# Performance work log

Measured on AMD Instinct MI355X. Metric: run time of the kernel, lower is better.

Reference implementation:

```python
import jax, jax.numpy as jnp
import numpy as np

NUM_HEADS = 4
NUM_GROUPS = 32
EPS = 1e-5

def setup_inputs() -> dict:
    key = jax.random.key(0)
    ks = jax.random.split(key, 3)
    B, C, H, W = 4, 256, 64, 64
    x = jax.random.normal(ks[0], (B, C, H, W), jnp.float32)
    gn_w = jnp.ones((C,), jnp.float32)
    gn_b = jnp.zeros((C,), jnp.float32)
    qkv_w = jax.random.normal(ks[1], (3 * C, C), jnp.float32) * 0.02
    qkv_b = jnp.zeros((3 * C,), jnp.float32)
    proj_w = jax.random.normal(ks[2], (C, C), jnp.float32) * 0.02
    proj_b = jnp.zeros((C,), jnp.float32)
    return dict(x=x, gn_w=gn_w, gn_b=gn_b, qkv_w=qkv_w, qkv_b=qkv_b,
                proj_w=proj_w, proj_b=proj_b)

def reference(x, gn_w, gn_b, qkv_w, qkv_b, proj_w, proj_b):
    B, C, H, W = x.shape
    n = H * W
    xf = x.reshape(B, C, n)
    # GroupNorm(32, C) over (channels-in-group, n)
    xg = xf.reshape(B, NUM_GROUPS, -1)
    mu = xg.mean(-1, keepdims=True)
    var = xg.var(-1, keepdims=True)
    xn = ((xg - mu) * jax.lax.rsqrt(var + EPS)).reshape(B, C, n)
    xn = xn * gn_w[None, :, None] + gn_b[None, :, None]
    # 1x1 conv QKV: [B, 3C, n]
    qkv = jnp.einsum('oc,bcn->bon', qkv_w, xn) + qkv_b[None, :, None]
    # head split exactly as torch: reshape(B*heads, 3C//heads, n) then chunk
    qkv = qkv.reshape(B * NUM_HEADS, 3 * C // NUM_HEADS, n)
    q, k, v = jnp.split(qkv, 3, axis=1)  # each [B*heads, head_dim, n]
    scale = (C // NUM_HEADS) ** -0.25
    w = jnp.einsum('bct,bcs->bts', q * scale, k * scale)  # [B*heads, n, n]
    w = jax.nn.softmax(w, axis=-1)
    h = jnp.einsum('bts,bcs->bct', w, v).reshape(B, C, n)
    h = jnp.einsum('oc,bcn->bon', proj_w, h) + proj_b[None, :, None]
    return x + h.reshape(B, C, H, W)
```

## Files before the change

### kernel.cpp

```cpp
#include <hip/hip_runtime.h>

typedef unsigned short u16;
typedef unsigned int u32;
typedef __bf16 bf16x8 __attribute__((ext_vector_type(8)));
typedef float f32x4 __attribute__((ext_vector_type(4)));
typedef u16 u16x4 __attribute__((ext_vector_type(4)));
typedef u16 u16x8 __attribute__((ext_vector_type(8)));

#define MFMA16x16x32(a, b, c) __builtin_amdgcn_mfma_f32_16x16x32_bf16((a), (b), (c), 0, 0, 0)

static constexpr int kB = 4;
static constexpr int kC = 256;
static constexpr int kN = 4096;
static constexpr int kHeads = 4;
static constexpr int kD = 64;
static constexpr int kSplit = 2;
static constexpr float kScale = 0.35355339059327373f;
static constexpr float kScaleQ = 0.51006971545f;

__device__ __forceinline__ u16 f2bf(float f) {
  union { float f; u32 i; } v; v.f = f;
  return (u16)((v.i + 0x7fffu + ((v.i >> 16) & 1u)) >> 16);
}
__device__ __forceinline__ bf16x8 ldb8(const u16* p) {
  return *reinterpret_cast<const bf16x8*>(p);
}
__device__ __forceinline__ float fast_exp2(float x) {
#if __has_builtin(__builtin_amdgcn_exp2f)
  return __builtin_amdgcn_exp2f(x);
#else
  float r;
  asm("v_exp_f32 %0, %1" : "=v"(r) : "v"(x));
  return r;
#endif
}

__global__ void convert_bf16(const float* __restrict__ in, u16* __restrict__ out,
                             int n) {
  for (int i = blockIdx.x * blockDim.x + threadIdx.x; i < n;
       i += gridDim.x * blockDim.x)
    out[i] = f2bf(in[i]);
}

__global__ __launch_bounds__(1024) void gn_kernel(const float* __restrict__ x,
                                                  const float* __restrict__ gnw,
                                                  const float* __restrict__ gnb,
                                                  u16* __restrict__ xnT) {
  const int g = blockIdx.x, b = blockIdx.y;
  const int tid = threadIdx.x;
  const float* xb = x + b * (kC * kN) + g * 8 * kN;
  float vals[4][8];
  float s = 0.f, ss = 0.f;
#pragma unroll
  for (int kk = 0; kk < 4; ++kk) {
    const int t = tid + kk * 1024;
#pragma unroll
    for (int c = 0; c < 8; ++c) {
      const float v_ = xb[c * kN + t];
      vals[kk][c] = v_;
      s += v_; ss += v_ * v_;
    }
  }
#pragma unroll
  for (int off = 32; off > 0; off >>= 1) {
    s += __shfl_down(s, off);
    ss += __shfl_down(ss, off);
  }
  __shared__ float rbuf[32];
  const int wid = tid >> 6, lane = tid & 63;
  if (lane == 0) { rbuf[wid] = s; rbuf[16 + wid] = ss; }
  __syncthreads();
  if (tid < 64) {
    float s2 = (lane < 16) ? rbuf[lane] : 0.f;
    float ss2 = (lane < 16) ? rbuf[16 + lane] : 0.f;
#pragma unroll
    for (int off = 8; off > 0; off >>= 1) {
      s2 += __shfl_down(s2, off);
      ss2 += __shfl_down(ss2, off);
    }
    if (lane == 0) { rbuf[0] = s2; rbuf[1] = ss2; }
  }
  __syncthreads();
  const float inv_n = 1.f / 32768.f;
  const float mu = rbuf[0] * inv_n;
  const float var = rbuf[1] * inv_n - mu * mu;
  const float rs = rsqrtf(var + 1e-5f);
  float wv[8], bv[8];
#pragma unroll
  for (int c = 0; c < 8; ++c) {
    const float wgt = gnw[g * 8 + c] * rs;
    wv[c] = wgt;
    bv[c] = gnb[g * 8 + c] - mu * wgt;
  }
  u16* ob = xnT + b * (kN * kC) + g * 8;
#pragma unroll
  for (int kk = 0; kk < 4; ++kk) {
    const int t = tid + kk * 1024;
    u16x8 pk;
#pragma unroll
    for (int c = 0; c < 8; ++c) pk[c] = f2bf(vals[kk][c] * wv[c] + bv[c]);
    *reinterpret_cast<u16x8*>(ob + t * kC) = pk;
  }
}

__global__ __launch_bounds__(256) void qkv_gemm(const u16* __restrict__ qkvw,
                                                const float* __restrict__ qkvb,
                                                const u16* __restrict__ xnT,
                                                u16* __restrict__ qt,
                                                u16* __restrict__ kt,
                                                u16* __restrict__ vv) {
  const int nblk = blockIdx.x, mblk = blockIdx.y, b = blockIdx.z;
  const int tid = threadIdx.x;
  const int w = tid >> 6, l = tid & 63, quad = l >> 4, col = l & 15;
  const int m0 = mblk * 64 + w * 16;
  const int n0 = nblk * 64;
  __shared__ __align__(16) u16 als[64 * 256];
  __shared__ __align__(16) u16 bls[64 * 256];
  {
    const u16* asrc = qkvw + (size_t)(mblk * 64) * kC;
    const u16* bsrc = xnT + (size_t)b * (kN * kC) + (size_t)n0 * kC;
#pragma unroll
    for (int p = 0; p < 8; ++p) {
      const int li = p * 256 + tid;
      const int row = li >> 5, ch = li & 31;
      const int sw = (ch ^ (row & 7)) * 8;
      *reinterpret_cast<bf16x8*>(&als[row * 256 + sw]) = ldb8(asrc + li * 8);
      *reinterpret_cast<bf16x8*>(&bls[row * 256 + sw]) = ldb8(bsrc + li * 8);
    }
  }
  __syncthreads();
  f32x4 acc[4] = {{0,0,0,0},{0,0,0,0},{0,0,0,0},{0,0,0,0}};
  const u16* arow = &als[(w * 16 + col) * 256];
  const int kx = col & 7;
#pragma unroll
  for (int ks = 0; ks < 8; ++ks) {
    const bf16x8 af = ldb8(arow + (((ks * 4 + quad) ^ kx)) * 8);
#pragma unroll
    for (int nt = 0; nt < 4; ++nt) {
      const bf16x8 bfr =
          ldb8(&bls[(nt * 16 + col) * 256 + (((ks * 4 + quad) ^ kx)) * 8]);
      acc[nt] = MFMA16x16x32(af, bfr, acc[nt]);
    }
  }
  const int o_base = m0 + quad * 4;
  const int head = o_base / 192;
  const int rr = o_base % 192;
  const int bh = b * kHeads + head;
  const int seg = rr >> 6;
  const int c0 = rr & 63;
  float bias[4];
#pragma unroll
  for (int r = 0; r < 4; ++r) bias[r] = qkvb[o_base + r];
  const float sc = (seg == 0) ? kScaleQ : kScale;
#pragma unroll
  for (int nt = 0; nt < 4; ++nt) {
    const int t = n0 + nt * 16 + col;
    if (seg == 2) {
      const int tp = n0 + (nt >> 1) * 32 + 8 * (col >> 2) + 4 * (nt & 1) + (col & 3);
#pragma unroll
      for (int r = 0; r < 4; ++r)
        vv[bh * (kD * kN) + (c0 + r) * kN + tp] = f2bf(acc[nt][r] + bias[r]);
    } else {
      u16* dst = (seg == 0 ? qt : kt) + bh * (kN * kD) + t * kD + c0;
      u16x4 pk;
#pragma unroll
      for (int r = 0; r < 4; ++r) pk[r] = f2bf((acc[nt][r] + bias[r]) * sc);
      *reinterpret_cast<u16x4*>(dst) = pk;
    }
  }
}

__global__ __launch_bounds__(256, 2) void attn_split(const u16* __restrict__ qt,
                                                     const u16* __restrict__ kt,
                                                     const u16* __restrict__ vv,
                                                     float* __restrict__ pO,
                                                     float* __restrict__ pl) {
  const int tblk = blockIdx.x, bh = blockIdx.y, z = blockIdx.z;
  const int tid = threadIdx.x;
  const int w = tid >> 6, l = tid & 63, quad = l >> 4, col = l & 15;
  const int t0 = tblk * 256 + w * 64;
  const u16* qb = qt + bh * (kN * kD);
  const u16* kb = kt + bh * (kN * kD);
  const u16* vb = vv + bh * (kD * kN);
  bf16x8 qf[4][2];
#pragma unroll
  for (int ti = 0; ti < 4; ++ti) {
    qf[ti][0] = ldb8(qb + (t0 + ti * 16 + col) * kD + quad * 8);
    qf[ti][1] = ldb8(qb + (t0 + ti * 16 + col) * kD + 32 + quad * 8);
  }
  u16x8 ones_u;
#pragma unroll
  for (int i = 0; i < 8; ++i) ones_u[i] = 0x3f80;
  const bf16x8 onesf = *reinterpret_cast<bf16x8*>(&ones_u);
  f32x4 oacc[4][4];
  f32x4 lacc[4];
#pragma unroll
  for (int ti = 0; ti < 4; ++ti) {
    lacc[ti] = f32x4{0, 0, 0, 0};
#pragma unroll
    for (int ct = 0; ct < 4; ++ct) oacc[ti][ct] = f32x4{0, 0, 0, 0};
  }

  __shared__ __align__(16) u16 kls[2][32][64];
  __shared__ __align__(16) u16 vls[2][32][64];
  constexpr int NIT = (kN / kSplit) / 32;
  const int s_beg = z * (kN / kSplit);

  const int srow = tid >> 3, sk8 = tid & 7, skey = srow & 7;
  const u16* ksrc = kb + (size_t)(s_beg + srow) * kD + sk8 * 8;
  u16* kdst = &kls[0][srow][((sk8 ^ skey)) * 8];
  const int sa = sk8 >> 2, sq = sk8 & 3;
  const u16* vsrc = vb + (size_t)(2 * srow + sa) * kN + s_beg + sq * 8;
  u16* vdst = &vls[0][srow][(((sa << 2) | sq) ^ skey) * 8];

  bf16x8 kstg = ldb8(ksrc);
  bf16x8 vstg = ldb8(vsrc);

#pragma unroll 2
  for (int it = 0; it < NIT; ++it) {
    const int cb = (it & 1) * (32 * 64);
    *reinterpret_cast<bf16x8*>(kdst + cb) = kstg;
    *reinterpret_cast<bf16x8*>(vdst + cb) = vstg;
    __syncthreads();
    if (it + 1 < NIT) {
      kstg = ldb8(ksrc + (size_t)(it + 1) * (32 * kD));
      vstg = ldb8(vsrc + (it + 1) * 32);
    }
    const u16* kl = &kls[0][0][0] + cb;
    const u16* vl = &vls[0][0][0] + cb;
    const int kx = (col & 7) * 8;
    const bf16x8 k00 = ldb8(kl + col * 64 + ((quad * 8) ^ kx));
    const bf16x8 k01 = ldb8(kl + col * 64 + ((32 + quad * 8) ^ kx));
    const bf16x8 k10 = ldb8(kl + (col + 16) * 64 + ((quad * 8) ^ kx));
    const bf16x8 k11 = ldb8(kl + (col + 16) * 64 + ((32 + quad * 8) ^ kx));
    bf16x8 vf[4];
    const int vslot = (((col & 1) << 2) | quad) ^ (col >> 1);
#pragma unroll
    for (int ct = 0; ct < 4; ++ct)
      vf[ct] = ldb8(vl + (ct * 8 + (col >> 1)) * 64 + vslot * 8);
#pragma unroll
    for (int ti = 0; ti < 4; ++ti) {
      f32x4 sa0 = {0, 0, 0, 0}, sa1 = {0, 0, 0, 0};
      sa0 = MFMA16x16x32(k00, qf[ti][0], sa0);
      sa0 = MFMA16x16x32(k01, qf[ti][1], sa0);
      sa1 = MFMA16x16x32(k10, qf[ti][0], sa1);
      sa1 = MFMA16x16x32(k11, qf[ti][1], sa1);
      const u32 e00 = __float_as_uint(fast_exp2(sa0[0]));
      const u32 e01 = __float_as_uint(fast_exp2(sa0[1]));
      const u32 e02 = __float_as_uint(fast_exp2(sa0[2]));
      const u32 e03 = __float_as_uint(fast_exp2(sa0[3]));
      const u32 e10 = __float_as_uint(fast_exp2(sa1[0]));
      const u32 e11 = __float_as_uint(fast_exp2(sa1[1]));
      const u32 e12 = __float_as_uint(fast_exp2(sa1[2]));
      const u32 e13 = __float_as_uint(fast_exp2(sa1[3]));
      union { u32 wd[4]; bf16x8 v; } pa;
      pa.wd[0] = __builtin_amdgcn_perm(e01, e00, 0x07060302u);
      pa.wd[1] = __builtin_amdgcn_perm(e03, e02, 0x07060302u);
      pa.wd[2] = __builtin_amdgcn_perm(e11, e10, 0x07060302u);
      pa.wd[3] = __builtin_amdgcn_perm(e13, e12, 0x07060302u);
#pragma unroll
      for (int ct = 0; ct < 4; ++ct)
        oacc[ti][ct] = MFMA16x16x32(pa.v, vf[ct], oacc[ti][ct]);
      lacc[ti] = MFMA16x16x32(pa.v, onesf, lacc[ti]);
    }
  }
  float* po = pO + (size_t)(z * 16 + bh) * kN * kD;
  float* plp = pl + (size_t)(z * 16 + bh) * kN;
#pragma unroll
  for (int ti = 0; ti < 4; ++ti)
#pragma unroll
    for (int r = 0; r < 4; ++r) {
      const int t = t0 + ti * 16 + quad * 4 + r;
#pragma unroll
      for (int ct = 0; ct < 4; ++ct)
        po[(size_t)t * kD + ct * 16 + col] = oacc[ti][ct][r];
      if (col == 0) plp[t] = lacc[ti][r];
    }
}

__global__ __launch_bounds__(256) void attn_combine(const float* __restrict__ pO,
                                                    const float* __restrict__ pl,
                                                    u16* __restrict__ ht) {
  const int idx = blockIdx.x * 256 + threadIdx.x;
  const int c0 = (idx & 15) * 4;
  const int t = (idx >> 4) & (kN - 1);
  const int bh = idx >> 16;
  f32x4 acc = {0, 0, 0, 0};
  float lsum = 0.f;
#pragma unroll
  for (int z = 0; z < kSplit; ++z) {
    const size_t base = ((size_t)(z * 16 + bh) * kN + t);
    acc += *reinterpret_cast<const f32x4*>(pO + base * kD + c0);
    lsum += pl[base];
  }
  const float inv = 1.f / lsum;
  u16x4 pk;
#pragma unroll
  for (int i = 0; i < 4; ++i) pk[i] = f2bf(acc[i] * inv);
  const int b = bh >> 2, head = bh & 3;
  *reinterpret_cast<u16x4*>(ht + (size_t)b * (kN * kC) + (size_t)t * kC +
                            head * kD + c0) = pk;
}

__global__ __launch_bounds__(256) void proj_kernel(const u16* __restrict__ projw,
                                                   const float* __restrict__ projb,
                                                   const u16* __restrict__ ht,
                                                   const float* __restrict__ x,
                                                   float* __restrict__ out) {
  const int nblk = blockIdx.x, mblk = blockIdx.y, b = blockIdx.z;
  const int tid = threadIdx.x;
  const int w = tid >> 6, l = tid & 63, quad = l >> 4, col = l & 15;
  const int m0 = mblk * 64 + w * 16;
  const int n0 = nblk * 64;
  __shared__ __align__(16) u16 als[64 * 256];
  __shared__ __align__(16) u16 bls[64 * 256];
  {
    const u16* asrc = projw + (size_t)(mblk * 64) * kC;
    const u16* bsrc = ht + (size_t)b * (kN * kC) + (size_t)n0 * kC;
#pragma unroll
    for (int p = 0; p < 8; ++p) {
      const int li = p * 256 + tid;
      const int row = li >> 5, ch = li & 31;
      const int sw = (ch ^ (row & 7)) * 8;
      *reinterpret_cast<bf16x8*>(&als[row * 256 + sw]) = ldb8(asrc + li * 8);
      *reinterpret_cast<bf16x8*>(&bls[row * 256 + sw]) = ldb8(bsrc + li * 8);
    }
  }
  __syncthreads();
  f32x4 acc[4] = {{0,0,0,0},{0,0,0,0},{0,0,0,0},{0,0,0,0}};
  const u16* arow = &als[(w * 16 + col) * 256];
  const int kx = col & 7;
#pragma unroll
  for (int ks = 0; ks < 8; ++ks) {
    const bf16x8 af = ldb8(arow + (((ks * 4 + quad) ^ kx)) * 8);
#pragma unroll
    for (int nt = 0; nt < 4; ++nt) {
      const bf16x8 bfr =
          ldb8(&bls[(nt * 16 + col) * 256 + (((ks * 4 + quad) ^ kx)) * 8]);
      acc[nt] = MFMA16x16x32(af, bfr, acc[nt]);
    }
  }
#pragma unroll
  for (int nt = 0; nt < 4; ++nt) {
    const int t = n0 + nt * 16 + col;
#pragma unroll
    for (int r = 0; r < 4; ++r) {
      const int o = m0 + quad * 4 + r;
      const int idx = b * (kC * kN) + o * kN + t;
      out[idx] = acc[nt][r] + projb[o] + x[idx];
    }
  }
}

extern "C" void kernel_launch(void* const* d_in, const int* in_sizes, int n_in,
                              void* d_out, int out_size, void* d_ws, size_t ws_size,
                              hipStream_t stream) {
  const float* x = (const float*)d_in[0];
  const float* gnw = (const float*)d_in[1];
  const float* gnb = (const float*)d_in[2];
  const float* qkvw_f = (const float*)d_in[3];
  const float* qkvb = (const float*)d_in[4];
  const float* projw_f = (const float*)d_in[5];
  const float* projb = (const float*)d_in[6];
  float* out = (float*)d_out;

  char* ws = (char*)d_ws;
  u16* xnT = (u16*)(ws);
  u16* qt = (u16*)(ws + (8u << 20));
  u16* kt = (u16*)(ws + (16u << 20));
  u16* vv = (u16*)(ws + (24u << 20));
  u16* ht = (u16*)(ws + (32u << 20));
  u16* qkvw = (u16*)(ws + (40u << 20));
  u16* projw = (u16*)(ws + (41u << 20));
  float* pO = (float*)(ws + (48u << 20));
  float* pl = (float*)(ws + (112u << 20));

  convert_bf16<<<dim3(192), dim3(256), 0, stream>>>(qkvw_f, qkvw, 768 * kC);
  convert_bf16<<<dim3(64), dim3(256), 0, stream>>>(projw_f, projw, kC * kC);
  gn_kernel<<<dim3(32, 4), dim3(1024), 0, stream>>>(x, gnw, gnb, xnT);
  qkv_gemm<<<dim3(64, 12, 4), dim3(256), 0, stream>>>(qkvw, qkvb, xnT, qt, kt, vv);
  attn_split<<<dim3(16, 16, kSplit), dim3(256), 0, stream>>>(qt, kt, vv, pO, pl);
  attn_combine<<<dim3(4096), dim3(256), 0, stream>>>(pO, pl, ht);
  proj_kernel<<<dim3(64, 4, 4), dim3(256), 0, stream>>>(projw, projb, ht, x, out);
}
```

Before: 192.9 us.

## Drop split-KV attention and combine kernel; normalize in-kernel with smaller query tiles

Removes the two-way key split and the separate combine kernel. Each attention block now covers 128 queries (32 per wave) over the full key range and writes normalized bf16 output directly to ht. The K/V tile per sync grows to 64 keys, and the two weight-conversion launches are merged into one. This avoids writing and re-reading the fp32 partial outputs and two launches, at the cost of halving per-wave query reuse of each loaded K/V tile.

```diff
diff --git a/kernel.cpp b/kernel.cpp
--- a/kernel.cpp
+++ b/kernel.cpp
@@ -14,7 +14,6 @@
 static constexpr int kN = 4096;
 static constexpr int kHeads = 4;
 static constexpr int kD = 64;
-static constexpr int kSplit = 2;
 static constexpr float kScale = 0.35355339059327373f;
 static constexpr float kScaleQ = 0.51006971545f;
 
@@ -35,11 +34,15 @@
 #endif
 }
 
-__global__ void convert_bf16(const float* __restrict__ in, u16* __restrict__ out,
-                             int n) {
-  for (int i = blockIdx.x * blockDim.x + threadIdx.x; i < n;
-       i += gridDim.x * blockDim.x)
-    out[i] = f2bf(in[i]);
+__global__ void convert_bf16_2(const float* __restrict__ in1, u16* __restrict__ out1,
+                               int n1, const float* __restrict__ in2,
+                               u16* __restrict__ out2, int n2) {
+  const int total = n1 + n2;
+  for (int i = blockIdx.x * blockDim.x + threadIdx.x; i < total;
+       i += gridDim.x * blockDim.x) {
+    if (i < n1) out1[i] = f2bf(in1[i]);
+    else out2[i - n1] = f2bf(in2[i - n1]);
+  }
 }
 
 __global__ __launch_bounds__(1024) void gn_kernel(const float* __restrict__ x,
@@ -173,18 +176,17 @@
 __global__ __launch_bounds__(256, 2) void attn_split(const u16* __restrict__ qt,
                                                      const u16* __restrict__ kt,
                                                      const u16* __restrict__ vv,
-                                                     float* __restrict__ pO,
-                                                     float* __restrict__ pl) {
-  const int tblk = blockIdx.x, bh = blockIdx.y, z = blockIdx.z;
+                                                     u16* __restrict__ ht) {
+  const int tblk = blockIdx.x, bh = blockIdx.y;
   const int tid = threadIdx.x;
   const int w = tid >> 6, l = tid & 63, quad = l >> 4, col = l & 15;
-  const int t0 = tblk * 256 + w * 64;
+  const int t0 = tblk * 128 + w * 32;
   const u16* qb = qt + bh * (kN * kD);
   const u16* kb = kt + bh * (kN * kD);
   const u16* vb = vv + bh * (kD * kN);
-  bf16x8 qf[4][2];
-#pragma unroll
-  for (int ti = 0; ti < 4; ++ti) {
+  bf16x8 qf[2][2];
+#pragma unroll
+  for (int ti = 0; ti < 2; ++ti) {
     qf[ti][0] = ldb8(qb + (t0 + ti * 16 + col) * kD + quad * 8);
     qf[ti][1] = ldb8(qb + (t0 + ti * 16 + col) * kD + 32 + quad * 8);
   }
@@ -192,114 +194,99 @@
 #pragma unroll
   for (int i = 0; i < 8; ++i) ones_u[i] = 0x3f80;
   const bf16x8 onesf = *reinterpret_cast<bf16x8*>(&ones_u);
-  f32x4 oacc[4][4];
-  f32x4 lacc[4];
-#pragma unroll
-  for (int ti = 0; ti < 4; ++ti) {
+  f32x4 oacc[2][4];
+  f32x4 lacc[2];
+#pragma unroll
+  for (int ti = 0; ti < 2; ++ti) {
     lacc[ti] = f32x4{0, 0, 0, 0};
 #pragma unroll
     for (int ct = 0; ct < 4; ++ct) oacc[ti][ct] = f32x4{0, 0, 0, 0};
   }
 
-  __shared__ __align__(16) u16 kls[2][32][64];
-  __shared__ __align__(16) u16 vls[2][32][64];
-  constexpr int NIT = (kN / kSplit) / 32;
-  const int s_beg = z * (kN / kSplit);
+  __shared__ __align__(16) u16 kls[2][2][32][64];
+  __shared__ __align__(16) u16 vls[2][2][32][64];
+  constexpr int NIT = kN / 64;
 
   const int srow = tid >> 3, sk8 = tid & 7, skey = srow & 7;
-  const u16* ksrc = kb + (size_t)(s_beg + srow) * kD + sk8 * 8;
-  u16* kdst = &kls[0][srow][((sk8 ^ skey)) * 8];
+  const u16* ksrc = kb + (size_t)srow * kD + sk8 * 8;
+  u16* kdst = &kls[0][0][srow][((sk8 ^ skey)) * 8];
   const int sa = sk8 >> 2, sq = sk8 & 3;
-  const u16* vsrc = vb + (size_t)(2 * srow + sa) * kN + s_beg + sq * 8;
-  u16* vdst = &vls[0][srow][(((sa << 2) | sq) ^ skey) * 8];
-
-  bf16x8 kstg = ldb8(ksrc);
-  bf16x8 vstg = ldb8(vsrc);
+  const u16* vsrc = vb + (size_t)(2 * srow + sa) * kN + sq * 8;
+  u16* vdst = &vls[0][0][srow][(((sa << 2) | sq) ^ skey) * 8];
+
+  bf16x8 kstg0 = ldb8(ksrc);
+  bf16x8 kstg1 = ldb8(ksrc + 32 * kD);
+  bf16x8 vstg0 = ldb8(vsrc);
+  bf16x8 vstg1 = ldb8(vsrc + 32);
 
 #pragma unroll 2
   for (int it = 0; it < NIT; ++it) {
-    const int cb = (it & 1) * (32 * 64);
-    *reinterpret_cast<bf16x8*>(kdst + cb) = kstg;
-    *reinterpret_cast<bf16x8*>(vdst + cb) = vstg;
+    const int cb = (it & 1) * (2 * 32 * 64);
+    *reinterpret_cast<bf16x8*>(kdst + cb) = kstg0;
+    *reinterpret_cast<bf16x8*>(kdst + cb + 2048) = kstg1;
+    *reinterpret_cast<bf16x8*>(vdst + cb) = vstg0;
+    *reinterpret_cast<bf16x8*>(vdst + cb + 2048) = vstg1;
     __syncthreads();
     if (it + 1 < NIT) {
-      kstg = ldb8(ksrc + (size_t)(it + 1) * (32 * kD));
-      vstg = ldb8(vsrc + (it + 1) * 32);
-    }
-    const u16* kl = &kls[0][0][0] + cb;
-    const u16* vl = &vls[0][0][0] + cb;
+      const size_t sb = (size_t)(it + 1) * 64;
+      kstg0 = ldb8(ksrc + sb * kD);
+      kstg1 = ldb8(ksrc + (sb + 32) * kD);
+      vstg0 = ldb8(vsrc + sb);
+      vstg1 = ldb8(vsrc + sb + 32);
+    }
     const int kx = (col & 7) * 8;
-    const bf16x8 k00 = ldb8(kl + col * 64 + ((quad * 8) ^ kx));
-    const bf16x8 k01 = ldb8(kl + col * 64 + ((32 + quad * 8) ^ kx));
-    const bf16x8 k10 = ldb8(kl + (col + 16) * 64 + ((quad * 8) ^ kx));
-    const bf16x8 k11 = ldb8(kl + (col + 16) * 64 + ((32 + quad * 8) ^ kx));
-    bf16x8 vf[4];
     const int vslot = (((col & 1) << 2) | quad) ^ (col >> 1);
 #pragma unroll
-    for (int ct = 0; ct < 4; ++ct)
-      vf[ct] = ldb8(vl + (ct * 8 + (col >> 1)) * 64 + vslot * 8);
-#pragma unroll
-    for (int ti = 0; ti < 4; ++ti) {
-      f32x4 sa0 = {0, 0, 0, 0}, sa1 = {0, 0, 0, 0};
-      sa0 = MFMA16x16x32(k00, qf[ti][0], sa0);
-      sa0 = MFMA16x16x32(k01, qf[ti][1], sa0);
-      sa1 = MFMA16x16x32(k10, qf[ti][0], sa1);
-      sa1 = MFMA16x16x32(k11, qf[ti][1], sa1);
-      const u32 e00 = __float_as_uint(fast_exp2(sa0[0]));
-      const u32 e01 = __float_as_uint(fast_exp2(sa0[1]));
-      const u32 e02 = __float_as_uint(fast_exp2(sa0[2]));
-      const u32 e03 = __float_as_uint(fast_exp2(sa0[3]));
-      const u32 e10 = __float_as_uint(fast_exp2(sa1[0]));
-      const u32 e11 = __float_as_uint(fast_exp2(sa1[1]));
-      const u32 e12 = __float_as_uint(fast_exp2(sa1[2]));
-      const u32 e13 = __float_as_uint(fast_exp2(sa1[3]));
-      union { u32 wd[4]; bf16x8 v; } pa;
-      pa.wd[0] = __builtin_amdgcn_perm(e01, e00, 0x07060302u);
-      pa.wd[1] = __builtin_amdgcn_perm(e03, e02, 0x07060302u);
-      pa.wd[2] = __builtin_amdgcn_perm(e11, e10, 0x07060302u);
-      pa.wd[3] = __builtin_amdgcn_perm(e13, e12, 0x07060302u);
+    for (int h = 0; h < 2; ++h) {
+      const u16* kl = &kls[0][0][0][0] + cb + h * 2048;
+      const u16* vl = &vls[0][0][0][0] + cb + h * 2048;
+      const bf16x8 k00 = ldb8(kl + col * 64 + ((quad * 8) ^ kx));
+      const bf16x8 k01 = ldb8(kl + col * 64 + ((32 + quad * 8) ^ kx));
+      const bf16x8 k10 = ldb8(kl + (col + 16) * 64 + ((quad * 8) ^ kx));
+      const bf16x8 k11 = ldb8(kl + (col + 16) * 64 + ((32 + quad * 8) ^ kx));
+      bf16x8 vf[4];
 #pragma unroll
       for (int ct = 0; ct < 4; ++ct)
-        oacc[ti][ct] = MFMA16x16x32(pa.v, vf[ct], oacc[ti][ct]);
-      lacc[ti] = MFMA16x16x32(pa.v, onesf, lacc[ti]);
-    }
-  }
-  float* po = pO + (size_t)(z * 16 + bh) * kN * kD;
-  float* plp = pl + (size_t)(z * 16 + bh) * kN;
-#pragma unroll
-  for (int ti = 0; ti < 4; ++ti)
+        vf[ct] = ldb8(vl + (ct * 8 + (col >> 1)) * 64 + vslot * 8);
+#pragma unroll
+      for (int ti = 0; ti < 2; ++ti) {
+        f32x4 sa0 = {0, 0, 0, 0}, sa1 = {0, 0, 0, 0};
+        sa0 = MFMA16x16x32(k00, qf[ti][0], sa0);
+        sa0 = MFMA16x16x32(k01, qf[ti][1], sa0);
+        sa1 = MFMA16x16x32(k10, qf[ti][0], sa1);
+        sa1 = MFMA16x16x32(k11, qf[ti][1], sa1);
+        const u32 e00 = __float_as_uint(fast_exp2(sa0[0]));
+        const u32 e01 = __float_as_uint(fast_exp2(sa0[1]));
+        const u32 e02 = __float_as_uint(fast_exp2(sa0[2]));
+        const u32 e03 = __float_as_uint(fast_exp2(sa0[3]));
+        const u32 e10 = __float_as_uint(fast_exp2(sa1[0]));
+        const u32 e11 = __float_as_uint(fast_exp2(sa1[1]));
+        const u32 e12 = __float_as_uint(fast_exp2(sa1[2]));
+        const u32 e13 = __float_as_uint(fast_exp2(sa1[3]));
+        union { u32 wd[4]; bf16x8 v; } pa;
+        pa.wd[0] = __builtin_amdgcn_perm(e01, e00, 0x07060302u);
+        pa.wd[1] = __builtin_amdgcn_perm(e03, e02, 0x07060302u);
+        pa.wd[2] = __builtin_amdgcn_perm(e11, e10, 0x07060302u);
+        pa.wd[3] = __builtin_amdgcn_perm(e13, e12, 0x07060302u);
+#pragma unroll
+        for (int ct = 0; ct < 4; ++ct)
+          oacc[ti][ct] = MFMA16x16x32(pa.v, vf[ct], oacc[ti][ct]);
+        lacc[ti] = MFMA16x16x32(pa.v, onesf, lacc[ti]);
+      }
+    }
+  }
+  const int b = bh >> 2, head = bh & 3;
+  u16* hb = ht + (size_t)b * (kN * kC) + head * kD;
+#pragma unroll
+  for (int ti = 0; ti < 2; ++ti)
 #pragma unroll
     for (int r = 0; r < 4; ++r) {
       const int t = t0 + ti * 16 + quad * 4 + r;
+      const float inv = 1.f / lacc[ti][r];
 #pragma unroll
       for (int ct = 0; ct < 4; ++ct)
-        po[(size_t)t * kD + ct * 16 + col] = oacc[ti][ct][r];
-      if (col == 0) plp[t] = lacc[ti][r];
-    }
-}
-
-__global__ __launch_bounds__(256) void attn_combine(const float* __restrict__ pO,
-                                                    const float* __restrict__ pl,
-                                                    u16* __restrict__ ht) {
-  const int idx = blockIdx.x * 256 + threadIdx.x;
-  const int c0 = (idx & 15) * 4;
-  const int t = (idx >> 4) & (kN - 1);
-  const int bh = idx >> 16;
-  f32x4 acc = {0, 0, 0, 0};
-  float lsum = 0.f;
-#pragma unroll
-  for (int z = 0; z < kSplit; ++z) {
-    const size_t base = ((size_t)(z * 16 + bh) * kN + t);
-    acc += *reinterpret_cast<const f32x4*>(pO + base * kD + c0);
-    lsum += pl[base];
-  }
-  const float inv = 1.f / lsum;
-  u16x4 pk;
-#pragma unroll
-  for (int i = 0; i < 4; ++i) pk[i] = f2bf(acc[i] * inv);
-  const int b = bh >> 2, head = bh & 3;
-  *reinterpret_cast<u16x4*>(ht + (size_t)b * (kN * kC) + (size_t)t * kC +
-                            head * kD + c0) = pk;
+        hb[(size_t)t * kC + ct * 16 + col] = f2bf(oacc[ti][ct][r] * inv);
+    }
 }
 
 __global__ __launch_bounds__(256) void proj_kernel(const u16* __restrict__ projw,
@@ -372,14 +359,11 @@
   u16* ht = (u16*)(ws + (32u << 20));
   u16* qkvw = (u16*)(ws + (40u << 20));
   u16* projw = (u16*)(ws + (41u << 20));
-  float* pO = (float*)(ws + (48u << 20));
-  float* pl = (float*)(ws + (112u << 20));
-
-  convert_bf16<<<dim3(192), dim3(256), 0, stream>>>(qkvw_f, qkvw, 768 * kC);
-  convert_bf16<<<dim3(64), dim3(256), 0, stream>>>(projw_f, projw, kC * kC);
+
+  convert_bf16_2<<<dim3(256), dim3(256), 0, stream>>>(qkvw_f, qkvw, 768 * kC,
+                                                      projw_f, projw, kC * kC);
   gn_kernel<<<dim3(32, 4), dim3(1024), 0, stream>>>(x, gnw, gnb, xnT);
   qkv_gemm<<<dim3(64, 12, 4), dim3(256), 0, stream>>>(qkvw, qkvb, xnT, qt, kt, vv);
-  attn_split<<<dim3(16, 16, kSplit), dim3(256), 0, stream>>>(qt, kt, vv, pO, pl);
-  attn_combine<<<dim3(4096), dim3(256), 0, stream>>>(pO, pl, ht);
+  attn_split<<<dim3(32, 16), dim3(256), 0, stream>>>(qt, kt, vv, ht);
   proj_kernel<<<dim3(64, 4, 4), dim3(256), 0, stream>>>(projw, projb, ht, x, out);
 }
```

New measurement: 188.6 us. -2.2%, faster.
